# Kernel optimization log

Hardware: AMD Instinct MI355X
Metric: run time of the kernel (lower is better)

## Reference

```python
import jax, jax.numpy as jnp
import numpy as np

B, S, D = 2, 2048, 2048
H, G = 16, 4
HD = D // H          # head_dim = 128
KV = HD * G          # 512


def setup_inputs() -> dict:
    key = jax.random.key(0)
    ks = jax.random.split(key, 5)
    scale = 1.0 / np.sqrt(D)
    return {
        "x": jax.random.normal(ks[0], (B, S, D), dtype=jnp.float32),
        "Wqkv": jax.random.normal(ks[1], (D, D + 2 * KV), dtype=jnp.float32) * scale,
        "bqkv": jax.random.normal(ks[2], (D + 2 * KV,), dtype=jnp.float32) * 0.01,
        "Wout": jax.random.normal(ks[3], (D, D), dtype=jnp.float32) * scale,
        "bout": jax.random.normal(ks[4], (D,), dtype=jnp.float32) * 0.01,
    }


def reference(x, Wqkv, bqkv, Wout, bout):
    b, s, _ = x.shape
    qkv = x @ Wqkv + bqkv                                  # [b, s, D + 2*KV]
    q, k, v = jnp.split(qkv, [D, D + KV], axis=-1)
    q = q.reshape(b, s, H, HD)                             # [b, s, H, hd]
    # torch .repeat tiles the group axis: head h -> group (h % G)
    k = jnp.tile(k.reshape(b, s, G, HD), (1, 1, H // G, 1))  # [b, s, H, hd]
    v = jnp.tile(v.reshape(b, s, G, HD), (1, 1, H // G, 1))
    # NOTE: original divides by head_dim (not sqrt(head_dim)) -- kept faithfully
    scores = jnp.einsum("bqhd,bkhd->bhqk", q, k) / HD      # [b, H, s, s]
    prob = jax.nn.softmax(scores, axis=-1)
    out = jnp.einsum("bhqk,bkhd->bqhd", prob, v).reshape(b, s, D)
    return out @ Wout + bout
```

## Files before the change

### kernel.cpp

```cpp
#include <hip/hip_runtime.h>
#include <stdint.h>

typedef __bf16 bf16;
typedef __bf16 bf16x8 __attribute__((ext_vector_type(8)));
typedef __bf16 bf16x4 __attribute__((ext_vector_type(4)));
typedef float  f32x4  __attribute__((ext_vector_type(4)));

#define B_   2
#define S_   2048
#define D_   2048
#define H_   16
#define G_   4
#define HD_  128
#define KV_  512
#define NQKV 3072
#define M_   4096

__device__ __forceinline__ void async16(bf16* lds, const bf16* g) {
  __builtin_amdgcn_global_load_lds(
      (const __attribute__((address_space(1))) unsigned int*)g,
      (__attribute__((address_space(3))) unsigned int*)lds, 16, 0, 0);
}

__device__ __forceinline__ f32x4 mfma16(bf16x8 a, bf16x8 b, f32x4 c) {
  return __builtin_amdgcn_mfma_f32_16x16x32_bf16(a, b, c, 0, 0, 0);
}

__global__ __launch_bounds__(256) void prep_kernel(const float* __restrict__ x,
                                                   const float* __restrict__ Wqkv,
                                                   const float* __restrict__ Wout,
                                                   bf16* __restrict__ xb,
                                                   bf16* __restrict__ wqkvT,
                                                   bf16* __restrict__ woutT) {
  __shared__ float tile[32][33];
  int bid = blockIdx.x;
  int t = threadIdx.x;

  if (bid < 8192) {
    int i = bid * 256 + t;
    float4 v = ((const float4*)x)[i];
    bf16x4 o = { (bf16)v.x, (bf16)v.y, (bf16)v.z, (bf16)v.w };
    *(bf16x4*)(xb + (size_t)i * 4) = o;
    return;
  }
  bid -= 8192;

  const float* src; bf16* dst; int rows, cols, nct;
  if (bid < 6144) { src = Wqkv; dst = wqkvT; rows = 2048; cols = 3072; nct = 96; }
  else { bid -= 6144; src = Wout; dst = woutT; rows = 2048; cols = 2048; nct = 64; }

  int bc = (bid % nct) * 32, br = (bid / nct) * 32;
  int tx = t & 31, ty = t >> 5;
  #pragma unroll
  for (int i = 0; i < 32; i += 8)
    tile[ty + i][tx] = src[(size_t)(br + ty + i) * cols + bc + tx];
  __syncthreads();
  #pragma unroll
  for (int i = 0; i < 32; i += 8)
    dst[(size_t)(bc + ty + i) * rows + br + tx] = (bf16)tile[tx][ty + i];
}

__global__ void transpose_v_kernel(const bf16* __restrict__ qkv,
                                   bf16* __restrict__ vt) {
  __shared__ bf16 tile[32][33];
  int bg = blockIdx.z; int b = bg / G_, g = bg % G_;
  int sb = blockIdx.x * 32, db = blockIdx.y * 32;
  int tx = threadIdx.x, ty = threadIdx.y;
  const bf16* src = qkv + (size_t)b * S_ * NQKV + (D_ + KV_ + g * HD_);
  #pragma unroll
  for (int i = 0; i < 32; i += 8)
    tile[ty + i][tx] = src[(size_t)(sb + ty + i) * NQKV + db + tx];
  __syncthreads();
  bf16* dst = vt + (size_t)(b * G_ + g) * HD_ * S_;
  #pragma unroll
  for (int i = 0; i < 32; i += 8)
    dst[(size_t)(db + ty + i) * S_ + sb + tx] = tile[tx][ty + i];
}

template <int OUT_BF16>
__global__ __launch_bounds__(256) void gemm_bt(const bf16* __restrict__ A,
                                               const bf16* __restrict__ Bt,
                                               const float* __restrict__ bias,
                                               void* __restrict__ Cout,
                                               int Ndim, int K) {
  __shared__ __align__(16) bf16 As[128 * 32];
  __shared__ __align__(16) bf16 Bs[128 * 32];
  int t = threadIdx.x;
  int w = t >> 6, l = t & 63, lr = l & 15, lg = l >> 4;
  int wm = w >> 1, wn = w & 1;
  int row0 = blockIdx.x * 128, col0 = blockIdx.y * 128;

  f32x4 acc[4][4] = {};

  const bf16* ga = A  + (size_t)(row0 + (t >> 2)) * K + (t & 3) * 8;
  const bf16* gb = Bt + (size_t)(col0 + (t >> 2)) * K + (t & 3) * 8;

  for (int k0 = 0; k0 < K; k0 += 32) {
    __syncthreads();
    #pragma unroll
    for (int i = 0; i < 2; i++)
      async16(&As[w * 512 + i * 2048], ga + (size_t)i * 64 * K + k0);
    #pragma unroll
    for (int i = 0; i < 2; i++)
      async16(&Bs[w * 512 + i * 2048], gb + (size_t)i * 64 * K + k0);
    __syncthreads();

    bf16x8 af[4], bfr[4];
    #pragma unroll
    for (int mi = 0; mi < 4; mi++)
      af[mi] = *(const bf16x8*)&As[(wm * 64 + mi * 16 + lr) * 32 + lg * 8];
    #pragma unroll
    for (int ni = 0; ni < 4; ni++)
      bfr[ni] = *(const bf16x8*)&Bs[(wn * 64 + ni * 16 + lr) * 32 + lg * 8];
    #pragma unroll
    for (int mi = 0; mi < 4; mi++)
      #pragma unroll
      for (int ni = 0; ni < 4; ni++)
        acc[mi][ni] = mfma16(af[mi], bfr[ni], acc[mi][ni]);
  }

  float bv[4];
  #pragma unroll
  for (int ni = 0; ni < 4; ni++)
    bv[ni] = bias[col0 + wn * 64 + ni * 16 + lr];

  #pragma unroll
  for (int mi = 0; mi < 4; mi++)
    #pragma unroll
    for (int ni = 0; ni < 4; ni++)
      #pragma unroll
      for (int r = 0; r < 4; r++) {
        int row = row0 + wm * 64 + mi * 16 + lg * 4 + r;
        int col = col0 + wn * 64 + ni * 16 + lr;
        float v = acc[mi][ni][r] + bv[ni];
        if (OUT_BF16)
          ((bf16*)Cout)[(size_t)row * Ndim + col] = (bf16)v;
        else
          ((float*)Cout)[(size_t)row * Ndim + col] = v;
      }
}

__global__ __launch_bounds__(256, 2) void attn_kernel(const bf16* __restrict__ qkv,
                                                      const bf16* __restrict__ vt,
                                                      bf16* __restrict__ attnb) {
  __shared__ __align__(16) bf16 Ks[2][64 * 128];
  __shared__ __align__(16) bf16 Vs[2][128 * 64];
  __shared__ __align__(16) bf16 Ps[4][32 * 64];

  int t = threadIdx.x, w = t >> 6, l = t & 63, lr = l & 15, lg = l >> 4;
  int rsw = lr & 7;
  int lin = blockIdx.x + gridDim.x * blockIdx.y;
  int swz = (lin & 7) * 64 + (lin >> 3);
  int q0 = (swz & 15) * 128;
  int hb2 = swz >> 4;
  int b = hb2 >> 4, gh = hb2 & 15;
  int g = gh >> 2, h = (gh & 3) * 4 + g;

  bf16x8 qf[2][4];
  #pragma unroll
  for (int mi = 0; mi < 2; mi++) {
    const bf16* qbase = qkv + (size_t)(b * S_ + q0 + w * 32 + mi * 16 + lr) * NQKV + h * HD_;
    #pragma unroll
    for (int kc = 0; kc < 4; kc++)
      qf[mi][kc] = *(const bf16x8*)(qbase + kc * 32 + lg * 8);
  }

  const bf16* kbase = qkv + (size_t)b * S_ * NQKV + D_ + g * HD_;
  const bf16* vbase = vt + (size_t)(b * G_ + g) * HD_ * S_;

  int krowi = w * 4 + (l >> 4);
  int ksw = (l & 15) ^ (krowi & 7);
  const bf16* kgl = kbase + (size_t)krowi * NQKV + ksw * 8;
  int vrowi = w * 8 + (l >> 3);
  int vsw = (l & 7) ^ ((l >> 3) & 7);
  const bf16* vgl = vbase + (size_t)vrowi * S_ + vsw * 8;

  auto STAGE_KV = [&](int nb, int kv0) {
    #pragma unroll
    for (int i = 0; i < 4; i++)
      async16(&Ks[nb][w * 512 + i * 2048], kgl + (size_t)(kv0 + i * 16) * NQKV);
    #pragma unroll
    for (int i = 0; i < 4; i++)
      async16(&Vs[nb][w * 512 + i * 2048], vgl + (size_t)(i * 32) * S_ + kv0);
  };

  float lsump[2] = {};
  f32x4 accO[2][8] = {};

  STAGE_KV(0, 0);

  for (int ti = 0; ti < S_ / 64; ++ti) {
    int cur = ti & 1;
    int kv0 = ti * 64;
    __syncthreads();
    if (ti + 1 < S_ / 64) STAGE_KV(cur ^ 1, kv0 + 64);

    const bf16* ks = &Ks[cur][0];
    const bf16* vs = &Vs[cur][0];
    bf16* psw = &Ps[w][0];

    __builtin_amdgcn_s_setprio(1);
    #pragma unroll
    for (int fk = 0; fk < 4; fk++) {
      bf16x8 kf[4];
      #pragma unroll
      for (int kc = 0; kc < 4; kc++)
        kf[kc] = *(const bf16x8*)&ks[(fk * 16 + lr) * 128 + (((kc * 4 + lg) ^ rsw) * 8)];
      f32x4 sacc[2] = {};
      #pragma unroll
      for (int mi = 0; mi < 2; mi++)
        #pragma unroll
        for (int kc = 0; kc < 4; kc++)
          sacc[mi] = mfma16(kf[kc], qf[mi][kc], sacc[mi]);
      #pragma unroll
      for (int mi = 0; mi < 2; mi++) {
        float p0 = __expf(sacc[mi][0] * 0.0078125f);
        float p1 = __expf(sacc[mi][1] * 0.0078125f);
        float p2 = __expf(sacc[mi][2] * 0.0078125f);
        float p3 = __expf(sacc[mi][3] * 0.0078125f);
        lsump[mi] += (p0 + p1) + (p2 + p3);
        bf16x4 pk = { (bf16)p0, (bf16)p1, (bf16)p2, (bf16)p3 };
        *(bf16x4*)&psw[(mi * 16 + lr) * 64 +
                       (((fk * 2 + (lg >> 1)) ^ rsw) * 8) + (lg & 1) * 4] = pk;
      }
    }
    __builtin_amdgcn_s_setprio(0);

    bf16x8 pa[2][2];
    #pragma unroll
    for (int mi = 0; mi < 2; mi++)
      #pragma unroll
      for (int kk = 0; kk < 2; kk++)
        pa[mi][kk] = *(const bf16x8*)&psw[(mi * 16 + lr) * 64 + (((kk * 4 + lg) ^ rsw) * 8)];

    __builtin_amdgcn_s_setprio(1);
    #pragma unroll
    for (int fd = 0; fd < 8; fd++) {
      bf16x8 vfr[2];
      #pragma unroll
      for (int kk = 0; kk < 2; kk++)
        vfr[kk] = *(const bf16x8*)&vs[(fd * 16 + lr) * 64 + (((kk * 4 + lg) ^ rsw) * 8)];
      #pragma unroll
      for (int mi = 0; mi < 2; mi++)
        #pragma unroll
        for (int kk = 0; kk < 2; kk++)
          accO[mi][fd] = mfma16(pa[mi][kk], vfr[kk], accO[mi][fd]);
    }
    __builtin_amdgcn_s_setprio(0);
  }

  #pragma unroll
  for (int mi = 0; mi < 2; mi++) {
    float s = lsump[mi];
    s += __shfl_xor(s, 16);
    s += __shfl_xor(s, 32);
    float rls[4];
    #pragma unroll
    for (int r = 0; r < 4; r++) rls[r] = 1.f / __shfl(s, lg * 4 + r);
    bf16* obase = attnb + (size_t)(b * S_ + q0 + w * 32 + mi * 16) * D_ + h * HD_;
    #pragma unroll
    for (int r = 0; r < 4; r++)
      #pragma unroll
      for (int fd = 0; fd < 8; fd++)
        obase[(size_t)(lg * 4 + r) * D_ + fd * 16 + lr] =
            (bf16)(accO[mi][fd][r] * rls[r]);
  }
}

extern "C" void kernel_launch(void* const* d_in, const int* in_sizes, int n_in,
                              void* d_out, int out_size, void* d_ws, size_t ws_size,
                              hipStream_t stream) {
  const float* x    = (const float*)d_in[0];
  const float* Wqkv = (const float*)d_in[1];
  const float* bqkv = (const float*)d_in[2];
  const float* Wout = (const float*)d_in[3];
  const float* bout = (const float*)d_in[4];
  float* out = (float*)d_out;

  char* p = (char*)d_ws;
  bf16* xb    = (bf16*)p; p += (size_t)M_ * D_ * 2;
  bf16* wqkvT = (bf16*)p; p += (size_t)NQKV * D_ * 2;
  bf16* woutT = (bf16*)p; p += (size_t)D_ * D_ * 2;
  bf16* qkvb  = (bf16*)p; p += (size_t)M_ * NQKV * 2;
  bf16* vtb   = (bf16*)p; p += (size_t)B_ * G_ * HD_ * S_ * 2;
  bf16* attnb = (bf16*)p; p += (size_t)M_ * D_ * 2;

  prep_kernel<<<dim3(8192 + 6144 + 4096), dim3(256), 0, stream>>>(
      x, Wqkv, Wout, xb, wqkvT, woutT);

  gemm_bt<1><<<dim3(M_ / 128, NQKV / 128), dim3(256), 0, stream>>>(xb, wqkvT, bqkv, (void*)qkvb, NQKV, D_);

  transpose_v_kernel<<<dim3(S_ / 32, HD_ / 32, B_ * G_), dim3(32, 8), 0, stream>>>(qkvb, vtb);

  attn_kernel<<<dim3(S_ / 128, B_ * H_), dim3(256), 0, stream>>>(qkvb, vtb, attnb);

  gemm_bt<0><<<dim3(M_ / 128, D_ / 128), dim3(256), 0, stream>>>(attnb, woutT, bout, (void*)out, D_, D_);
}
```

Baseline: 217.9 us.

## Replace GEMM with triple-buffered 256-row tile kernel with swizzled LDS and grid remap

Replaces the simple single-buffered 128x128 GEMM with a 512-thread kernel that uses 256xBN tiles and a three-stage async global-to-LDS pipeline. Loads for the next stages are interleaved with MFMA phases under split barriers, with explicit vmcnt waits and raised wave priority around the MFMA blocks. LDS columns are XOR-swizzled to avoid bank conflicts, and block indices are remapped for L2 locality. This is meant to hide global load latency and raise MFMA utilisation for both projection GEMMs. In exchange it uses more LDS and registers, and correctness depends on hand-tuned waitcnt counts.

Measured after the change: 246.8 us. +13.3%, slower.

```diff
diff --git a/kernel.cpp b/kernel.cpp
--- a/kernel.cpp
+++ b/kernel.cpp
@@ -77,46 +77,93 @@
     dst[(size_t)(db + ty + i) * S_ + sb + tx] = tile[tx][ty + i];
 }
 
-template <int OUT_BF16>
-__global__ __launch_bounds__(256) void gemm_bt(const bf16* __restrict__ A,
-                                               const bf16* __restrict__ Bt,
-                                               const float* __restrict__ bias,
-                                               void* __restrict__ Cout,
-                                               int Ndim, int K) {
-  __shared__ __align__(16) bf16 As[128 * 32];
-  __shared__ __align__(16) bf16 Bs[128 * 32];
-  int t = threadIdx.x;
-  int w = t >> 6, l = t & 63, lr = l & 15, lg = l >> 4;
-  int wm = w >> 1, wn = w & 1;
-  int row0 = blockIdx.x * 128, col0 = blockIdx.y * 128;
-
-  f32x4 acc[4][4] = {};
-
-  const bf16* ga = A  + (size_t)(row0 + (t >> 2)) * K + (t & 3) * 8;
-  const bf16* gb = Bt + (size_t)(col0 + (t >> 2)) * K + (t & 3) * 8;
-
-  for (int k0 = 0; k0 < K; k0 += 32) {
-    __syncthreads();
-    #pragma unroll
-    for (int i = 0; i < 2; i++)
-      async16(&As[w * 512 + i * 2048], ga + (size_t)i * 64 * K + k0);
-    #pragma unroll
-    for (int i = 0; i < 2; i++)
-      async16(&Bs[w * 512 + i * 2048], gb + (size_t)i * 64 * K + k0);
-    __syncthreads();
-
-    bf16x8 af[4], bfr[4];
-    #pragma unroll
-    for (int mi = 0; mi < 4; mi++)
-      af[mi] = *(const bf16x8*)&As[(wm * 64 + mi * 16 + lr) * 32 + lg * 8];
-    #pragma unroll
-    for (int ni = 0; ni < 4; ni++)
-      bfr[ni] = *(const bf16x8*)&Bs[(wn * 64 + ni * 16 + lr) * 32 + lg * 8];
-    #pragma unroll
-    for (int mi = 0; mi < 4; mi++)
-      #pragma unroll
-      for (int ni = 0; ni < 4; ni++)
-        acc[mi][ni] = mfma16(af[mi], bfr[ni], acc[mi][ni]);
+template <int BN_, int OUT_BF16>
+__global__ __launch_bounds__(512, 2) void gemm_p3(const bf16* __restrict__ A,
+                                                  const bf16* __restrict__ Bt,
+                                                  const float* __restrict__ bias,
+                                                  void* __restrict__ Cout,
+                                                  int Ndim, int K, int nbm) {
+  constexpr int WN    = BN_ / 64;
+  constexpr int WAVEM = 256 / (8 / WN);
+  constexpr int MFR   = WAVEM / 16;
+  constexpr int MPP   = MFR / 4;
+  constexpr int NIS   = 2 + BN_ / 128;
+
+  __shared__ __align__(16) bf16 Asb[3][256 * 32];
+  __shared__ __align__(16) bf16 Bsb[3][BN_ * 32];
+
+  int t = threadIdx.x, w = t >> 6, l = t & 63, lr = l & 15, lg = l >> 4;
+  int wm = w / WN, wn = w % WN;
+  int rsw4 = lr & 3;
+
+  int cpx = (int)gridDim.x >> 3;
+  int swz = ((int)blockIdx.x & 7) * cpx + ((int)blockIdx.x >> 3);
+  int row0 = (swz % nbm) * 256, col0 = (swz / nbm) * BN_;
+
+  int r8 = w * 16 + (l >> 2);
+  int csw = (l & 3) ^ (r8 & 3);
+  const bf16* gA = A  + (size_t)(row0 + r8) * K + csw * 8;
+  const bf16* gB = Bt + (size_t)(col0 + r8) * K + csw * 8;
+
+  auto stage_issue = [&](int buf, int kt, int p) {
+    size_t ko = (size_t)kt * 32;
+    if (p < 2)
+      async16(&Asb[buf][p * 4096 + w * 512], gA + (size_t)(p * 128) * K + ko);
+    else
+      async16(&Bsb[buf][(p - 2) * 4096 + w * 512], gB + (size_t)((p - 2) * 128) * K + ko);
+  };
+
+#define LDA(mi) (*(const bf16x8*)&as[(wm * WAVEM + (mi) * 16 + lr) * 32 + ((lg ^ rsw4) * 8)])
+#define LDB(ni) (*(const bf16x8*)&bs[(wn * 64 + (ni) * 16 + lr) * 32 + ((lg ^ rsw4) * 8)])
+
+  const int NT = K >> 5;
+  f32x4 acc[MFR][4] = {};
+
+  #pragma unroll
+  for (int p = 0; p < NIS; p++) stage_issue(0, 0, p);
+  #pragma unroll
+  for (int p = 0; p < NIS; p++) stage_issue(1, 1, p);
+
+  for (int kt = 0; kt < NT; ++kt) {
+    if (kt + 1 < NT) {
+      if constexpr (NIS == 4) asm volatile("s_waitcnt vmcnt(4)" ::: "memory");
+      else                    asm volatile("s_waitcnt vmcnt(3)" ::: "memory");
+    } else {
+      asm volatile("s_waitcnt vmcnt(0)" ::: "memory");
+    }
+    __builtin_amdgcn_sched_barrier(0);
+    __builtin_amdgcn_s_barrier();
+    __builtin_amdgcn_sched_barrier(0);
+
+    const bf16* as = &Asb[kt % 3][0];
+    const bf16* bs = &Bsb[kt % 3][0];
+    int bufn = (kt + 2) % 3;
+    bool t2ok = (kt + 2) < NT;
+
+    bf16x8 bfr[4];
+    #pragma unroll
+    for (int p = 0; p < 4; p++) {
+      if (p == 0) {
+        #pragma unroll
+        for (int ni = 0; ni < 4; ni++) bfr[ni] = LDB(ni);
+      }
+      bf16x8 af[MPP];
+      #pragma unroll
+      for (int m2 = 0; m2 < MPP; m2++) af[m2] = LDA(p * MPP + m2);
+      if (t2ok) { if (p < NIS) stage_issue(bufn, kt + 2, p); }
+      __builtin_amdgcn_s_setprio(1);
+      #pragma unroll
+      for (int m2 = 0; m2 < MPP; m2++)
+        #pragma unroll
+        for (int ni = 0; ni < 4; ni++)
+          acc[p * MPP + m2][ni] = mfma16(af[m2], bfr[ni], acc[p * MPP + m2][ni]);
+      __builtin_amdgcn_s_setprio(0);
+      if (p < 3) {
+        __builtin_amdgcn_sched_barrier(0);
+        __builtin_amdgcn_s_barrier();
+        __builtin_amdgcn_sched_barrier(0);
+      }
+    }
   }
 
   float bv[4];
@@ -125,12 +172,12 @@
     bv[ni] = bias[col0 + wn * 64 + ni * 16 + lr];
 
   #pragma unroll
-  for (int mi = 0; mi < 4; mi++)
+  for (int mi = 0; mi < MFR; mi++)
     #pragma unroll
     for (int ni = 0; ni < 4; ni++)
       #pragma unroll
       for (int r = 0; r < 4; r++) {
-        int row = row0 + wm * 64 + mi * 16 + lg * 4 + r;
+        int row = row0 + wm * WAVEM + mi * 16 + lg * 4 + r;
         int col = col0 + wn * 64 + ni * 16 + lr;
         float v = acc[mi][ni][r] + bv[ni];
         if (OUT_BF16)
@@ -138,6 +185,8 @@
         else
           ((float*)Cout)[(size_t)row * Ndim + col] = v;
       }
+#undef LDA
+#undef LDB
 }
 
 __global__ __launch_bounds__(256, 2) void attn_kernel(const bf16* __restrict__ qkv,
@@ -288,11 +337,13 @@
   prep_kernel<<<dim3(8192 + 6144 + 4096), dim3(256), 0, stream>>>(
       x, Wqkv, Wout, xb, wqkvT, woutT);
 
-  gemm_bt<1><<<dim3(M_ / 128, NQKV / 128), dim3(256), 0, stream>>>(xb, wqkvT, bqkv, (void*)qkvb, NQKV, D_);
+  gemm_p3<256, 1><<<dim3((M_ / 256) * (NQKV / 256)), dim3(512), 0, stream>>>(
+      xb, wqkvT, bqkv, (void*)qkvb, NQKV, D_, M_ / 256);
 
   transpose_v_kernel<<<dim3(S_ / 32, HD_ / 32, B_ * G_), dim3(32, 8), 0, stream>>>(qkvb, vtb);
 
   attn_kernel<<<dim3(S_ / 128, B_ * H_), dim3(256), 0, stream>>>(qkvb, vtb, attnb);
 
-  gemm_bt<0><<<dim3(M_ / 128, D_ / 128), dim3(256), 0, stream>>>(attnb, woutT, bout, (void*)out, D_, D_);
-}
+  gemm_p3<128, 0><<<dim3((M_ / 256) * (D_ / 128)), dim3(512), 0, stream>>>(
+      attnb, woutT, bout, (void*)out, D_, D_, M_ / 256);
+}
```
